# Performance work log

Measured on AMD Instinct MI355X. Metric: run time of the kernel, lower is better.

## Reference

```python
import jax, jax.numpy as jnp
import numpy as np

N_EMBD = 2048
N_Q = 32
N_KV = 8
GROUP = N_Q // N_KV   # 4
HD = N_EMBD // N_Q    # 64
BASE = 10000.0
NEG_INF = -1e30


def _rope(x):
    """Rotate-half RoPE on last dim; positions 1..t along dim -2 (as in the
    original _build_cache which uses arange(1, seq_len+1))."""
    t, d = x.shape[-2], x.shape[-1]
    d2 = d // 2
    theta = 1.0 / (BASE ** (jnp.arange(0, d, 2, dtype=jnp.float32) / d))  # (d/2,)
    pos = jnp.arange(1, t + 1, dtype=jnp.float32)                          # (t,)
    ang = pos[:, None] * theta[None, :]                                    # (t, d/2)
    ang = jnp.concatenate([ang, ang], axis=-1)                             # (t, d)
    sin, cos = jnp.sin(ang), jnp.cos(ang)
    rot = jnp.concatenate([-x[..., d2:], x[..., :d2]], axis=-1)
    return x * cos + rot * sin


def setup_inputs() -> dict:
    key = jax.random.key(0)
    ks = jax.random.split(key, 5)
    b, t = 2, 1024
    s = 1.0 / np.sqrt(N_EMBD)
    return {
        "x": jax.random.normal(ks[0], (b, t, N_EMBD), dtype=jnp.float32),
        "wq": jax.random.normal(ks[1], (N_EMBD, N_EMBD), dtype=jnp.float32) * s,
        "bq": jnp.zeros((N_EMBD,), dtype=jnp.float32),
        "wk": jax.random.normal(ks[2], (N_EMBD, N_KV * HD), dtype=jnp.float32) * s,
        "bk": jnp.zeros((N_KV * HD,), dtype=jnp.float32),
        "wv": jax.random.normal(ks[3], (N_EMBD, N_KV * HD), dtype=jnp.float32) * s,
        "bv": jnp.zeros((N_KV * HD,), dtype=jnp.float32),
        "wo": jax.random.normal(ks[4], (N_EMBD, N_EMBD), dtype=jnp.float32) * s,
        "bo": jnp.zeros((N_EMBD,), dtype=jnp.float32),
    }


def reference(x, wq, bq, wk, bk, wv, bv, wo, bo):
    b, t, _ = x.shape
    q = x @ wq + bq                                   # (b, t, E)
    k = x @ wk + bk                                   # (b, t, NKV*HD)
    v = x @ wv + bv
    q = q.reshape(b, t, N_Q, HD).transpose(0, 2, 1, 3)        # (b, nq, t, d)
    q = q.reshape(b, N_KV, GROUP, t, HD)                      # (b, hkv, g, t, d)
    k = k.reshape(b, t, N_KV, HD).transpose(0, 2, 1, 3)       # (b, hkv, t, d)
    v = v.reshape(b, t, N_KV, HD).transpose(0, 2, 1, 3)
    q = _rope(q)
    k = _rope(k)
    scale = jnp.sqrt(jnp.float32(HD))
    att = jnp.einsum("bhgqd,bhkd->bhgqk", q, k) / scale       # (b, hkv, g, t, t)
    causal = jnp.tril(jnp.ones((t, t), dtype=bool))
    att = jnp.where(causal, att, NEG_INF)
    att = jax.nn.softmax(att, axis=-1)
    out = jnp.einsum("bhgqk,bhkd->bhgqd", att, v)             # (b, hkv, g, t, d)
    out = out.transpose(0, 3, 1, 2, 4).reshape(b, t, N_EMBD)  # (b, t, E)
    return out @ wo + bo
```

## Files before the change

### kernel.cpp

```cpp
#include <hip/hip_runtime.h>
#include <hip/hip_bf16.h>
#include <cstdint>


typedef __attribute__((ext_vector_type(8))) short short8;
typedef __attribute__((ext_vector_type(4))) short short4v;
typedef __attribute__((ext_vector_type(4))) float f32x4;

__device__ inline short f2b(float f) {
  union { float f; unsigned u; } v; v.f = f;
  unsigned r = v.u + 0x7fffu + ((v.u >> 16) & 1u);
  return (short)(r >> 16);
}

__device__ inline float exp2_fast(float x) {
  float r;
  asm("v_exp_f32 %0, %1" : "=v"(r) : "v"(x));
  return r;
}

__device__ inline void gl_lds16(const void* g, void* l) {
  __builtin_amdgcn_global_load_lds((const __attribute__((address_space(1))) void*)g,
                                   (__attribute__((address_space(3))) void*)l,
                                   16, 0, 0);
}

__global__ void prep_all(const float* __restrict__ x, const float* __restrict__ wq,
                         const float* __restrict__ wk, const float* __restrict__ wv,
                         const float* __restrict__ wo, short* __restrict__ xb,
                         short* __restrict__ WqkvT, short* __restrict__ woT, int n4) {
  __shared__ float tile[64][65];
  const int bx = blockIdx.x;
  const int tid = threadIdx.x;
  if (bx >= 80) {
    int i = ((bx - 80) * 32 + blockIdx.y) * 256 + tid;
    if (i < n4) {
      float4 v = ((const float4*)x)[i];
      short4v o; o.x = f2b(v.x); o.y = f2b(v.y); o.z = f2b(v.z); o.w = f2b(v.w);
      ((short4v*)xb)[i] = o;
    }
    return;
  }
  const float* W; short* WT; int N, off, nb;
  if (bx < 32)      { W = wq; WT = WqkvT; N = 2048; off = 0;    nb = bx * 64; }
  else if (bx < 40) { W = wk; WT = WqkvT; N = 512;  off = 2048; nb = (bx - 32) * 64; }
  else if (bx < 48) { W = wv; WT = WqkvT; N = 512;  off = 2560; nb = (bx - 40) * 64; }
  else              { W = wo; WT = woT;   N = 2048; off = 0;    nb = (bx - 48) * 64; }
  const int kb = blockIdx.y * 64;
  const int c = tid & 63, r0 = tid >> 6;
#pragma unroll
  for (int s = 0; s < 16; ++s) {
    int k = r0 + s * 4;
    tile[c][k] = W[(size_t)(kb + k) * N + nb + c];
  }
  __syncthreads();
#pragma unroll
  for (int s = 0; s < 16; ++s) {
    int n = r0 + s * 4;
    WT[(size_t)(off + nb + n) * 2048 + kb + c] = f2b(tile[n][c]);
  }
}

__device__ __forceinline__ void gemm_loop_bk64(const short* __restrict__ Ag,
                                               const short* __restrict__ Bg,
                                               short* lA, short* lB,
                                               int w, int l15, int q4,
                                               f32x4 acc[2][4]) {
  const int K = 2048, NS = 32;
  const int q4x = q4 ^ ((l15 >> 1) & 3);
  auto stage = [&](int s, int d) {
    const short* As = Ag + s * 64;
    const short* Bs = Bg + s * 64;
    short* a = lA + d * 8192 + w * 512;
    gl_lds16(As, a);
    gl_lds16(As + 64 * K, a + 2048);
    gl_lds16(As + 32, a + 4096);
    gl_lds16(As + 64 * K + 32, a + 6144);
    short* bp = lB + d * 4096 + w * 512;
    gl_lds16(Bs, bp);
    gl_lds16(Bs + 32, bp + 2048);
  };
  stage(0, 0);
  for (int s = 0; s < NS; ++s) {
    const int d = s & 1;
    __syncthreads();
    if (s + 1 < NS) stage(s + 1, d ^ 1);
#pragma unroll
    for (int ks = 0; ks < 2; ++ks) {
      const short* ap = lA + d * 8192 + ks * 4096;
      const short* bp = lB + d * 4096 + ks * 2048;
      short8 af[2], bf[4];
#pragma unroll
      for (int mf = 0; mf < 2; ++mf) af[mf] = *(const short8*)(ap + (w * 32 + mf * 16 + l15) * 32 + q4x * 8);
#pragma unroll
      for (int nf = 0; nf < 4; ++nf) bf[nf] = *(const short8*)(bp + (nf * 16 + l15) * 32 + q4x * 8);
#pragma unroll
      for (int mf = 0; mf < 2; ++mf)
#pragma unroll
        for (int nf = 0; nf < 4; ++nf)
          acc[mf][nf] = __builtin_amdgcn_mfma_f32_16x16x32_bf16(af[mf], bf[nf], acc[mf][nf], 0, 0, 0);
    }
  }
}

__launch_bounds__(256, 3)
__global__ void gemm_qkv(const short* __restrict__ A, const short* __restrict__ BT,
                         const float* __restrict__ bq, const float* __restrict__ bk,
                         const float* __restrict__ bv,
                         short* __restrict__ Qb, short* __restrict__ Kb,
                         short* __restrict__ VTb) {
  __shared__ __align__(16) short lA[16384];
  __shared__ __align__(16) short lB[8192];
  const int K = 2048;
  const int tid = threadIdx.x, lane = tid & 63, w = tid >> 6;
  const int q4 = lane >> 4, l15 = lane & 15;
  const int bn = blockIdx.x * 64, bm = blockIdx.y * 128;

  const int swzc = ((tid & 3) ^ ((tid >> 3) & 3)) << 3;
  const short* Ag = A + (size_t)(bm + (tid >> 2)) * K + swzc;
  const short* Bg = BT + (size_t)(bn + (tid >> 2)) * K + swzc;

  f32x4 acc[2][4];
  const f32x4 fz = {0.f, 0.f, 0.f, 0.f};
#pragma unroll
  for (int i = 0; i < 2; ++i)
#pragma unroll
    for (int j = 0; j < 4; ++j) acc[i][j] = fz;

  gemm_loop_bk64(Ag, Bg, lA, lB, w, l15, q4, acc);

  const float L2T = 0.4152410118609203f;
  const float theta_a = exp2_fast(-(float)l15 * L2T);
  const float theta_b = exp2_fast(-(float)(l15 + 16) * L2T);
  const float s2 = 0.18033688011112042f;

  if (bn < 2048) {
    const int h = bn >> 6;
    float bb0 = bq[bn + l15], bb1 = bq[bn + 16 + l15], bb2 = bq[bn + 32 + l15], bb3 = bq[bn + 48 + l15];
#pragma unroll
    for (int mf = 0; mf < 2; ++mf)
#pragma unroll
      for (int r = 0; r < 4; ++r) {
        int row = bm + w * 32 + mf * 16 + q4 * 4 + r;
        int batch = row >> 10, t = row & 1023;
        float pos = (float)(t + 1);
        float sa, ca, sb, cb;
        __sincosf(pos * theta_a, &sa, &ca);
        __sincosf(pos * theta_b, &sb, &cb);
        float x0 = acc[mf][0][r] + bb0, x2 = acc[mf][2][r] + bb2;
        float x1 = acc[mf][1][r] + bb1, x3 = acc[mf][3][r] + bb3;
        size_t base = ((size_t)(batch * 32 + h) * 1024 + t) * 64;
        Qb[base + l15]      = f2b((x0 * ca - x2 * sa) * s2);
        Qb[base + l15 + 32] = f2b((x2 * ca + x0 * sa) * s2);
        Qb[base + l15 + 16] = f2b((x1 * cb - x3 * sb) * s2);
        Qb[base + l15 + 48] = f2b((x3 * cb + x1 * sb) * s2);
      }
  } else if (bn < 2560) {
    const int co = bn - 2048;
    const int hkv = co >> 6;
    float bb0 = bk[co + l15], bb1 = bk[co + 16 + l15], bb2 = bk[co + 32 + l15], bb3 = bk[co + 48 + l15];
#pragma unroll
    for (int mf = 0; mf < 2; ++mf)
#pragma unroll
      for (int r = 0; r < 4; ++r) {
        int row = bm + w * 32 + mf * 16 + q4 * 4 + r;
        int batch = row >> 10, t = row & 1023;
        float pos = (float)(t + 1);
        float sa, ca, sb, cb;
        __sincosf(pos * theta_a, &sa, &ca);
        __sincosf(pos * theta_b, &sb, &cb);
        float x0 = acc[mf][0][r] + bb0, x2 = acc[mf][2][r] + bb2;
        float x1 = acc[mf][1][r] + bb1, x3 = acc[mf][3][r] + bb3;
        size_t base = (size_t)(batch * 8 + hkv) * 65536 + t * 32;
        Kb[base + l15]              = f2b(x0 * ca - x2 * sa);
        Kb[base + l15 + 16]         = f2b(x1 * cb - x3 * sb);
        Kb[base + 32768 + l15]      = f2b(x2 * ca + x0 * sa);
        Kb[base + 32768 + l15 + 16] = f2b(x3 * cb + x1 * sb);
      }
  } else {
    const int co = bn - 2560;
    const int hkv = co >> 6;
    float bb[4];
#pragma unroll
    for (int nf = 0; nf < 4; ++nf) bb[nf] = bv[co + nf * 16 + l15];
    const int batch = (bm + w * 32) >> 10;
    const size_t vbase = (size_t)(batch * 8 + hkv) * 65536;
#pragma unroll
    for (int mf = 0; mf < 2; ++mf) {
      const int t0 = (bm + w * 32 + mf * 16 + q4 * 4) & 1023;
      const size_t rbase = vbase + (size_t)(t0 >> 5) * 2048 + (t0 & 31);
#pragma unroll
      for (int nf = 0; nf < 4; ++nf) {
        short4v pk;
#pragma unroll
        for (int r = 0; r < 4; ++r) pk[r] = f2b(acc[mf][nf][r] + bb[nf]);
        *(short4v*)(VTb + rbase + (nf * 16 + l15) * 32) = pk;
      }
    }
  }
}

#define PROW 72
__launch_bounds__(256, 2)
__global__ void attn10_kernel(const short* __restrict__ Qb, const short* __restrict__ Kb,
                              const short* __restrict__ VTb, short* __restrict__ AO) {
  __shared__ __align__(16) short lK[2 * 4096];
  __shared__ __align__(16) short lV[3 * 4096];
  __shared__ __align__(16) short lP[2][4][16 * PROW];
  const int tid = threadIdx.x, lane = tid & 63, w = tid >> 6;
  const int q4 = lane >> 4, l15 = lane & 15;
  const int q4x = q4 ^ ((l15 >> 1) & 3);
  const int swzc = ((tid & 3) ^ ((tid >> 3) & 3)) << 3;
  const int pr = blockIdx.x;
  const int jA = pr, jB = 15 - pr;
  const int nsA = jA + 1;
  const int h = blockIdx.y, b = blockIdx.z;
  const int hkv = h >> 2;

  const short* Qg = Qb + (size_t)(b * 32 + h) * 65536;
  const short* Kg = Kb + (size_t)(b * 8 + hkv) * 65536;
  const short* Vg = VTb + (size_t)(b * 8 + hkv) * 65536;

  short8 qfA0, qfA1, qfB0, qfB1;
  {
    const short* qr = Qg + (size_t)(jA * 64 + w * 16 + l15) * 64 + q4 * 8;
    qfA0 = *(const short8*)(qr); qfA1 = *(const short8*)(qr + 32);
    const short* qr2 = Qg + (size_t)(jB * 64 + w * 16 + l15) * 64 + q4 * 8;
    qfB0 = *(const short8*)(qr2); qfB1 = *(const short8*)(qr2 + 32);
  }

  const f32x4 fz = {0.f, 0.f, 0.f, 0.f};
  f32x4 o[4], ol;
  short8 ones;
#pragma unroll
  for (int i = 0; i < 8; ++i) ones[i] = (short)0x3F80;
  ol = fz;
#pragma unroll
  for (int dt = 0; dt < 4; ++dt) o[dt] = fz;

  auto stage = [&](int s) {
    const int kt = (s < nsA) ? s : s - nsA;
    const short* Ksrc = Kg + (size_t)(kt * 64 + (tid >> 2)) * 32 + swzc;
    short* kd = lK + (s & 1) * 4096 + w * 512;
    gl_lds16(Ksrc, kd);
    gl_lds16(Ksrc + 32768, kd + 2048);
    const short* Vsrc = Vg + (size_t)(2 * kt) * 2048 + (tid >> 2) * 32 + swzc;
    short* vd = lV + (s % 3) * 4096 + w * 512;
    gl_lds16(Vsrc, vd);
    gl_lds16(Vsrc + 2048, vd + 2048);
  };

  auto qk = [&](int s) {
    const int inA = (s < nsA);
    const int jt = inA ? jA : jB;
    const int kt = inA ? s : s - nsA;
    const short8 qf0 = inA ? qfA0 : qfB0;
    const short8 qf1 = inA ? qfA1 : qfB1;
    const short* kp = lK + (s & 1) * 4096;
    short8 kf0[4], kf1[4];
#pragma unroll
    for (int nt = 0; nt < 4; ++nt) {
      kf0[nt] = *(const short8*)(kp + (nt * 16 + l15) * 32 + q4x * 8);
      kf1[nt] = *(const short8*)(kp + 2048 + (nt * 16 + l15) * 32 + q4x * 8);
    }
    f32x4 sv[4];
#pragma unroll
    for (int nt = 0; nt < 4; ++nt) {
      f32x4 z = __builtin_amdgcn_mfma_f32_16x16x32_bf16(qf0, kf0[nt], fz, 0, 0, 0);
      sv[nt] = __builtin_amdgcn_mfma_f32_16x16x32_bf16(qf1, kf1[nt], z, 0, 0, 0);
    }
    if (kt == jt) {
#pragma unroll
      for (int r = 0; r < 4; ++r) {
        const int qrow = jt * 64 + w * 16 + q4 * 4 + r;
        const int col = kt * 64 + l15;
#pragma unroll
        for (int nt = 0; nt < 4; ++nt)
          if (col + nt * 16 > qrow) sv[nt][r] = -1e30f;
      }
    }
    short* lPm = lP[s & 1][w];
#pragma unroll
    for (int r = 0; r < 4; ++r)
#pragma unroll
      for (int nt = 0; nt < 4; ++nt)
        lPm[(q4 * 4 + r) * PROW + nt * 16 + l15] = f2b(exp2_fast(sv[nt][r] - 16.f));
  };

  auto pv = [&](int sp) {
    const short* vp = lV + (sp % 3) * 4096;
    const short* lPm = lP[sp & 1][w];
    short8 vf0[4], vf1[4];
#pragma unroll
    for (int dt = 0; dt < 4; ++dt) {
      vf0[dt] = *(const short8*)(vp + (dt * 16 + l15) * 32 + q4x * 8);
      vf1[dt] = *(const short8*)(vp + 2048 + (dt * 16 + l15) * 32 + q4x * 8);
    }
    short8 pf0 = *(const short8*)(lPm + l15 * PROW + q4 * 8);
    short8 pf1 = *(const short8*)(lPm + l15 * PROW + 32 + q4 * 8);
    ol = __builtin_amdgcn_mfma_f32_16x16x32_bf16(pf0, ones, ol, 0, 0, 0);
    ol = __builtin_amdgcn_mfma_f32_16x16x32_bf16(pf1, ones, ol, 0, 0, 0);
#pragma unroll
    for (int dt = 0; dt < 4; ++dt) {
      o[dt] = __builtin_amdgcn_mfma_f32_16x16x32_bf16(pf0, vf0[dt], o[dt], 0, 0, 0);
      o[dt] = __builtin_amdgcn_mfma_f32_16x16x32_bf16(pf1, vf1[dt], o[dt], 0, 0, 0);
    }
  };

  auto emit = [&](int jt) {
#pragma unroll
    for (int r = 0; r < 4; ++r) {
      float inv = __builtin_amdgcn_rcpf(ol[r]);
      int row = jt * 64 + w * 16 + q4 * 4 + r;
#pragma unroll
      for (int dt = 0; dt < 4; ++dt)
        AO[(size_t)(b * 1024 + row) * 2048 + h * 64 + dt * 16 + l15] = f2b(o[dt][r] * inv);
    }
  };

  stage(0);
  for (int s = 0; s < 17; ++s) {
    __syncthreads();
    if (s + 1 < 17) stage(s + 1);
    qk(s);
    if (s > 0) {
      pv(s - 1);
      if (s - 1 == nsA - 1) {
        emit(jA);
        ol = fz;
#pragma unroll
        for (int dt = 0; dt < 4; ++dt) o[dt] = fz;
      }
    }
  }
  pv(16);
  emit(jB);
}

__launch_bounds__(256, 3)
__global__ void gemm_out(const short* __restrict__ A, const short* __restrict__ BT,
                         float* __restrict__ C, const float* __restrict__ bias,
                         int N, int K) {
  __shared__ __align__(16) short lA[16384];
  __shared__ __align__(16) short lB[8192];
  const int tid = threadIdx.x, lane = tid & 63, w = tid >> 6;
  const int q4 = lane >> 4, l15 = lane & 15;
  const int bn = blockIdx.x * 64, bm = blockIdx.y * 128;

  const int swzc = ((tid & 3) ^ ((tid >> 3) & 3)) << 3;
  const short* Ag = A + (size_t)(bm + (tid >> 2)) * K + swzc;
  const short* Bg = BT + (size_t)(bn + (tid >> 2)) * K + swzc;

  f32x4 acc[2][4];
  const f32x4 fz = {0.f, 0.f, 0.f, 0.f};
#pragma unroll
  for (int i = 0; i < 2; ++i)
#pragma unroll
    for (int j = 0; j < 4; ++j) acc[i][j] = fz;

  gemm_loop_bk64(Ag, Bg, lA, lB, w, l15, q4, acc);

#pragma unroll
  for (int mf = 0; mf < 2; ++mf)
#pragma unroll
    for (int nf = 0; nf < 4; ++nf) {
      int col = bn + nf * 16 + l15;
      float bb = bias[col];
#pragma unroll
      for (int r = 0; r < 4; ++r) {
        int row = bm + w * 32 + mf * 16 + q4 * 4 + r;
        C[(size_t)row * N + col] = acc[mf][nf][r] + bb;
      }
    }
}

extern "C" void kernel_launch(void* const* d_in, const int* in_sizes, int n_in,
                              void* d_out, int out_size, void* d_ws, size_t ws_size,
                              hipStream_t stream) {
  const float* x  = (const float*)d_in[0];
  const float* wq = (const float*)d_in[1];
  const float* bq = (const float*)d_in[2];
  const float* wk = (const float*)d_in[3];
  const float* bk = (const float*)d_in[4];
  const float* wv = (const float*)d_in[5];
  const float* bv = (const float*)d_in[6];
  const float* wo = (const float*)d_in[7];
  const float* bo = (const float*)d_in[8];
  float* out = (float*)d_out;
  const int B = in_sizes[0] / (1024 * 2048);
  const int M = B * 1024;

  char* ws = (char*)d_ws;
  size_t off = 0;
  auto alloc = [&](size_t bytes) -> char* {
    char* p = ws + off;
    off += (bytes + 255) & ~(size_t)255;
    return p;
  };
  short* xb    = (short*)alloc((size_t)M * 2048 * 2);
  short* WqkvT = (short*)alloc((size_t)3072 * 2048 * 2);
  short* woT   = (short*)alloc((size_t)2048 * 2048 * 2);
  short* Qb    = (short*)alloc((size_t)B * 32 * 1024 * 64 * 2);
  short* Kb    = (short*)alloc((size_t)B * 8 * 2 * 1024 * 32 * 2);
  short* VTb   = (short*)alloc((size_t)B * 8 * 32 * 64 * 32 * 2);
  short* AO    = (short*)alloc((size_t)M * 2048 * 2);

  const int n4 = M * 2048 / 4;
  const int nbc = (n4 + 255) / 256;
  prep_all<<<dim3(80 + (nbc + 31) / 32, 32), 256, 0, stream>>>(x, wq, wk, wv, wo, xb, WqkvT, woT, n4);
  gemm_qkv<<<dim3(48, M / 128), 256, 0, stream>>>(xb, WqkvT, bq, bk, bv, Qb, Kb, VTb);
  attn10_kernel<<<dim3(8, 32, B), 256, 0, stream>>>(Qb, Kb, VTb, AO);
  gemm_out<<<dim3(32, M / 128), 256, 0, stream>>>(AO, woT, out, bo, 2048, 2048);
}
```

Baseline: 196.3 us.

## Load GEMM A operand directly from global into registers, bypassing LDS

```diff
diff --git a/kernel.cpp b/kernel.cpp
--- a/kernel.cpp
+++ b/kernel.cpp
@@ -61,55 +61,61 @@
   }
 }
 
-__device__ __forceinline__ void gemm_loop_bk64(const short* __restrict__ Ag,
-                                               const short* __restrict__ Bg,
-                                               short* lA, short* lB,
-                                               int w, int l15, int q4,
-                                               f32x4 acc[2][4]) {
+__device__ __forceinline__ void gemm_loop_v2(const short* __restrict__ A,
+                                             const short* __restrict__ Bg,
+                                             short* lB,
+                                             int bm, int w, int l15, int q4,
+                                             f32x4 acc[2][4]) {
   const int K = 2048, NS = 32;
   const int q4x = q4 ^ ((l15 >> 1) & 3);
-  auto stage = [&](int s, int d) {
-    const short* As = Ag + s * 64;
+  const short* Ar0 = A + (size_t)(bm + w * 32 + l15) * K + q4 * 8;
+  const short* Ar1 = Ar0 + 16 * K;
+
+  auto stageB = [&](int s, int d) {
     const short* Bs = Bg + s * 64;
-    short* a = lA + d * 8192 + w * 512;
-    gl_lds16(As, a);
-    gl_lds16(As + 64 * K, a + 2048);
-    gl_lds16(As + 32, a + 4096);
-    gl_lds16(As + 64 * K + 32, a + 6144);
     short* bp = lB + d * 4096 + w * 512;
     gl_lds16(Bs, bp);
     gl_lds16(Bs + 32, bp + 2048);
   };
-  stage(0, 0);
+  short8 a0[2], a1[2], n0[2], n1[2];
+  auto loadA = [&](int s, short8* f0, short8* f1) {
+    f0[0] = *(const short8*)(Ar0 + s * 64);
+    f0[1] = *(const short8*)(Ar0 + s * 64 + 32);
+    f1[0] = *(const short8*)(Ar1 + s * 64);
+    f1[1] = *(const short8*)(Ar1 + s * 64 + 32);
+  };
+
+  loadA(0, a0, a1);
+  stageB(0, 0);
   for (int s = 0; s < NS; ++s) {
     const int d = s & 1;
     __syncthreads();
-    if (s + 1 < NS) stage(s + 1, d ^ 1);
+    if (s + 1 < NS) { stageB(s + 1, d ^ 1); loadA(s + 1, n0, n1); }
 #pragma unroll
     for (int ks = 0; ks < 2; ++ks) {
-      const short* ap = lA + d * 8192 + ks * 4096;
       const short* bp = lB + d * 4096 + ks * 2048;
-      short8 af[2], bf[4];
-#pragma unroll
-      for (int mf = 0; mf < 2; ++mf) af[mf] = *(const short8*)(ap + (w * 32 + mf * 16 + l15) * 32 + q4x * 8);
+      short8 bf[4];
 #pragma unroll
       for (int nf = 0; nf < 4; ++nf) bf[nf] = *(const short8*)(bp + (nf * 16 + l15) * 32 + q4x * 8);
-#pragma unroll
-      for (int mf = 0; mf < 2; ++mf)
-#pragma unroll
-        for (int nf = 0; nf < 4; ++nf)
-          acc[mf][nf] = __builtin_amdgcn_mfma_f32_16x16x32_bf16(af[mf], bf[nf], acc[mf][nf], 0, 0, 0);
-    }
-  }
-}
-
-__launch_bounds__(256, 3)
+      const short8 af0 = ks ? a0[1] : a0[0];
+      const short8 af1 = ks ? a1[1] : a1[0];
+#pragma unroll
+      for (int nf = 0; nf < 4; ++nf) {
+        acc[0][nf] = __builtin_amdgcn_mfma_f32_16x16x32_bf16(af0, bf[nf], acc[0][nf], 0, 0, 0);
+        acc[1][nf] = __builtin_amdgcn_mfma_f32_16x16x32_bf16(af1, bf[nf], acc[1][nf], 0, 0, 0);
+      }
+    }
+#pragma unroll
+    for (int ks = 0; ks < 2; ++ks) { a0[ks] = n0[ks]; a1[ks] = n1[ks]; }
+  }
+}
+
+__launch_bounds__(256, 4)
 __global__ void gemm_qkv(const short* __restrict__ A, const short* __restrict__ BT,
                          const float* __restrict__ bq, const float* __restrict__ bk,
                          const float* __restrict__ bv,
                          short* __restrict__ Qb, short* __restrict__ Kb,
                          short* __restrict__ VTb) {
-  __shared__ __align__(16) short lA[16384];
   __shared__ __align__(16) short lB[8192];
   const int K = 2048;
   const int tid = threadIdx.x, lane = tid & 63, w = tid >> 6;
@@ -117,7 +123,6 @@
   const int bn = blockIdx.x * 64, bm = blockIdx.y * 128;
 
   const int swzc = ((tid & 3) ^ ((tid >> 3) & 3)) << 3;
-  const short* Ag = A + (size_t)(bm + (tid >> 2)) * K + swzc;
   const short* Bg = BT + (size_t)(bn + (tid >> 2)) * K + swzc;
 
   f32x4 acc[2][4];
@@ -127,7 +132,7 @@
 #pragma unroll
     for (int j = 0; j < 4; ++j) acc[i][j] = fz;
 
-  gemm_loop_bk64(Ag, Bg, lA, lB, w, l15, q4, acc);
+  gemm_loop_v2(A, Bg, lB, bm, w, l15, q4, acc);
 
   const float L2T = 0.4152410118609203f;
   const float theta_a = exp2_fast(-(float)l15 * L2T);
@@ -337,18 +342,16 @@
   emit(jB);
 }
 
-__launch_bounds__(256, 3)
+__launch_bounds__(256, 4)
 __global__ void gemm_out(const short* __restrict__ A, const short* __restrict__ BT,
                          float* __restrict__ C, const float* __restrict__ bias,
                          int N, int K) {
-  __shared__ __align__(16) short lA[16384];
   __shared__ __align__(16) short lB[8192];
   const int tid = threadIdx.x, lane = tid & 63, w = tid >> 6;
   const int q4 = lane >> 4, l15 = lane & 15;
   const int bn = blockIdx.x * 64, bm = blockIdx.y * 128;
 
   const int swzc = ((tid & 3) ^ ((tid >> 3) & 3)) << 3;
-  const short* Ag = A + (size_t)(bm + (tid >> 2)) * K + swzc;
   const short* Bg = BT + (size_t)(bn + (tid >> 2)) * K + swzc;
 
   f32x4 acc[2][4];
@@ -358,7 +361,7 @@
 #pragma unroll
     for (int j = 0; j < 4; ++j) acc[i][j] = fz;
 
-  gemm_loop_bk64(Ag, Bg, lA, lB, w, l15, q4, acc);
+  gemm_loop_v2(A, Bg, lB, bm, w, l15, q4, acc);
 
 #pragma unroll
   for (int mf = 0; mf < 2; ++mf)
```

After: 223.6 us. 1.14x slower.
